# Performance work log

Hardware: AMD Instinct MI355X
Metric: run time of the kernel (lower is better)

The kernel has to match this reference:

```python
import jax, jax.numpy as jnp
import numpy as np

MARGIN = 1.0


def setup_inputs() -> dict:
    key = jax.random.key(0)
    k1, k2 = jax.random.split(key)
    N, D, C = 8192, 128, 64
    embeddings = jax.random.normal(k1, (N, D), dtype=jnp.float32)
    labels = jax.random.randint(k2, (N,), 0, C, dtype=jnp.int64)
    return {"embeddings": embeddings, "labels": labels}


def _pairwise_euclidean(x):
    # ||xi - xj|| via Gram trick; safe sqrt (zero grad at 0, matches masked use)
    sq = jnp.sum(x * x, axis=1)                      # [N]
    d2 = sq[:, None] + sq[None, :] - 2.0 * (x @ x.T)  # [N, N]
    d2 = jnp.maximum(d2, 0.0)
    pos = d2 > 0.0
    return jnp.where(pos, jnp.sqrt(jnp.where(pos, d2, 1.0)), 0.0)


def reference(embeddings, labels):
    N = embeddings.shape[0]
    dist = _pairwise_euclidean(embeddings)            # [N, N]
    same = labels[:, None] == labels[None, :]         # [N, N]
    eye = jnp.eye(N, dtype=bool)
    pos_mask = same & ~eye
    neg_mask = ~same

    neg_inf = jnp.float32(-jnp.inf)
    pos_inf = jnp.float32(jnp.inf)
    hardest_pos = jnp.max(jnp.where(pos_mask, dist, neg_inf), axis=1)  # [N]
    hardest_neg = jnp.min(jnp.where(neg_mask, dist, pos_inf), axis=1)  # [N]

    has_pos = jnp.any(pos_mask, axis=1)
    has_neg = jnp.any(neg_mask, axis=1)
    tl = jax.nn.relu(hardest_pos - hardest_neg + MARGIN)               # [N]
    valid = has_pos & has_neg & (tl > 0.0)

    total = jnp.sum(jnp.where(valid, tl, 0.0))
    count = jnp.sum(valid)
    return jnp.where(count > 0, total / jnp.maximum(count, 1).astype(total.dtype), jnp.float32(0.0))
```

## Files before the change

### kernel.cpp

```cpp
#include <hip/hip_runtime.h>
#include <hip/hip_bf16.h>
#include <math.h>

#define NN 8192
#define DD 128
#define BM 256
#define BN 64
#define NPART 16
#define JRANGE (NN / NPART)
#define NTILES (JRANGE / BN)

typedef __attribute__((ext_vector_type(8))) short bf16x8;
typedef __attribute__((ext_vector_type(4))) float f32x4;

#define WS_SJC 0
#define WS_HPK 65536
#define WS_HNK (WS_HPK + NN * 4)
#define WS_AB  (WS_HNK + NN * 4)

__device__ __forceinline__ unsigned fkey(float f) {
    unsigned u = __float_as_uint(f);
    return (u & 0x80000000u) ? ~u : (u | 0x80000000u);
}
__device__ __forceinline__ float fkey_inv(unsigned k) {
    unsigned u = (k & 0x80000000u) ? (k ^ 0x80000000u) : ~k;
    return __uint_as_float(u);
}
__device__ __forceinline__ ushort f2bf(float x) {
    __hip_bfloat16 h = __float2bfloat16(x);
    return *reinterpret_cast<ushort*>(&h);
}

__global__ __launch_bounds__(256)
void prepq_k(const float* __restrict__ emb, const int* __restrict__ lab,
             float2* __restrict__ sjc, unsigned* __restrict__ hpK,
             unsigned* __restrict__ hnK, ushort* __restrict__ aB) {
    const int lane = threadIdx.x & 63;
    const int w    = threadIdx.x >> 6;
    const int half = lane >> 5;
    const int l32  = lane & 31;
    const int row  = blockIdx.x * 8 + w * 2 + half;

    float4 v = reinterpret_cast<const float4*>(emb)[row * 32 + l32];
    float s = 0.f;
    s = fmaf(v.x, v.x, s); s = fmaf(v.y, v.y, s);
    s = fmaf(v.z, v.z, s); s = fmaf(v.w, v.w, s);
#pragma unroll
    for (int off = 1; off < 32; off <<= 1) s += __shfl_xor(s, off, 64);

    ushort4 b;
    b.x = f2bf(v.x); b.y = f2bf(v.y); b.z = f2bf(v.z); b.w = f2bf(v.w);
    const int idx = (row >> 4) * 2048 + (l32 >> 3) * 512 + ((l32 >> 1) & 3) * 128
                  + (row & 15) * 8 + (l32 & 1) * 4;
    *reinterpret_cast<ushort4*>(aB + idx) = b;

    if (l32 == 0) sjc[row] = make_float2(s, __int_as_float(lab[row]));
    if (threadIdx.x < 8) {
        int r0 = blockIdx.x * 8 + threadIdx.x;
        hpK[r0] = 0x007FFFFFu;
        hnK[r0] = 0xFF800000u;
    }
}

__global__ __launch_bounds__(256, 2)
void hardest_k(const ushort* __restrict__ aB, const float2* __restrict__ sjc,
               unsigned* __restrict__ hpK, unsigned* __restrict__ hnK) {
    const int tid  = threadIdx.x;
    const int w    = tid >> 6;
    const int lane = tid & 63;
    const int lrow = lane & 15;
    const int lk   = lane >> 4;
    const int ib   = (int)blockIdx.x >> 4;
    const int part = (int)blockIdx.x & 15;
    const int i0   = ib * BM;
    const int jbeg = part * JRANGE;

    bf16x8 a[4][4];
#pragma unroll
    for (int s = 0; s < 4; ++s) {
        const int gA = ib * 16 + w * 4 + s;
#pragma unroll
        for (int q = 0; q < 4; ++q)
            a[s][q] = *reinterpret_cast<const bf16x8*>(&aB[gA * 2048 + q * 512 + lane * 8]);
    }
    int   li[4][4];
    float hpg[4][4], hng[4][4];
#pragma unroll
    for (int s = 0; s < 4; ++s)
#pragma unroll
        for (int t = 0; t < 4; ++t) {
            float2 md = sjc[i0 + w * 64 + s * 16 + lk * 4 + t];
            li[s][t]  = __float_as_int(md.y);
            hpg[s][t] = -INFINITY;
            hng[s][t] =  INFINITY;
        }

#pragma unroll 2
    for (int jt = 0; jt < NTILES; ++jt) {
        const int j0 = jbeg + jt * BN;
#pragma unroll
        for (int c = 0; c < 4; ++c) {
            const int gB = (j0 >> 4) + c;
            const ushort* bp = &aB[gB * 2048 + lane * 8];
            bf16x8 b0 = *reinterpret_cast<const bf16x8*>(bp);
            bf16x8 b1 = *reinterpret_cast<const bf16x8*>(bp + 512);
            bf16x8 b2 = *reinterpret_cast<const bf16x8*>(bp + 1024);
            bf16x8 b3 = *reinterpret_cast<const bf16x8*>(bp + 1536);
            float2 sv = sjc[j0 + c * 16 + lrow];
            f32x4 acc[4];
            f32x4 zero = {0.f, 0.f, 0.f, 0.f};
#pragma unroll
            for (int s = 0; s < 4; ++s) acc[s] = zero;
            __builtin_amdgcn_s_setprio(1);
#pragma unroll
            for (int s = 0; s < 4; ++s) {
                acc[s] = __builtin_amdgcn_mfma_f32_16x16x32_bf16(a[s][0], b0, acc[s], 0, 0, 0);
                acc[s] = __builtin_amdgcn_mfma_f32_16x16x32_bf16(a[s][1], b1, acc[s], 0, 0, 0);
                acc[s] = __builtin_amdgcn_mfma_f32_16x16x32_bf16(a[s][2], b2, acc[s], 0, 0, 0);
                acc[s] = __builtin_amdgcn_mfma_f32_16x16x32_bf16(a[s][3], b3, acc[s], 0, 0, 0);
            }
            __builtin_amdgcn_s_setprio(0);
            const float sqj = sv.x;
            const int   lj  = __float_as_int(sv.y);
#pragma unroll
            for (int s = 0; s < 4; ++s)
#pragma unroll
                for (int t = 0; t < 4; ++t) {
                    float gg = fmaf(-2.f, acc[s][t], sqj);
                    bool same = (li[s][t] == lj);
                    hpg[s][t] = fmaxf(hpg[s][t], same ? gg : -INFINITY);
                    hng[s][t] = fminf(hng[s][t], same ? INFINITY : gg);
                }
        }
    }

#pragma unroll
    for (int off = 1; off < 16; off <<= 1)
#pragma unroll
        for (int s = 0; s < 4; ++s)
#pragma unroll
            for (int t = 0; t < 4; ++t) {
                hpg[s][t] = fmaxf(hpg[s][t], __shfl_xor(hpg[s][t], off, 64));
                hng[s][t] = fminf(hng[s][t], __shfl_xor(hng[s][t], off, 64));
            }
    if (lrow == 0) {
#pragma unroll
        for (int s = 0; s < 4; ++s)
#pragma unroll
            for (int t = 0; t < 4; ++t) {
                int i = i0 + w * 64 + s * 16 + lk * 4 + t;
                atomicMax(&hpK[i], fkey(hpg[s][t]));
                atomicMin(&hnK[i], fkey(hng[s][t]));
            }
    }
}

__global__ __launch_bounds__(1024)
void final_k(const unsigned* __restrict__ hpK, const unsigned* __restrict__ hnK,
             const float2* __restrict__ sjc, float* __restrict__ out) {
    float total = 0.f, cnt = 0.f;
    for (int i = threadIdx.x; i < NN; i += 1024) {
        float hp = fkey_inv(hpK[i]);
        float hn = fkey_inv(hnK[i]);
        float s  = sjc[i].x;
        float hp2 = s + hp, hn2 = s + hn;
        float hpd = (hp2 == -INFINITY) ? -INFINITY : sqrtf(fmaxf(hp2, 0.f));
        float hnd = (hn2 ==  INFINITY) ?  INFINITY : sqrtf(fmaxf(hn2, 0.f));
        float tl = hpd - hnd + 1.0f;
        if (tl > 0.f) { total += tl; cnt += 1.f; }
    }
#pragma unroll
    for (int off = 1; off < 64; off <<= 1) {
        total += __shfl_xor(total, off, 64);
        cnt   += __shfl_xor(cnt,   off, 64);
    }
    __shared__ float sT[16], sC[16];
    int wave = threadIdx.x >> 6;
    if ((threadIdx.x & 63) == 0) { sT[wave] = total; sC[wave] = cnt; }
    __syncthreads();
    if (threadIdx.x == 0) {
        float T = 0.f, Cn = 0.f;
#pragma unroll
        for (int k = 0; k < 16; ++k) { T += sT[k]; Cn += sC[k]; }
        out[0] = (Cn > 0.f) ? T / Cn : 0.f;
    }
}

extern "C" void kernel_launch(void* const* d_in, const int* in_sizes, int n_in,
                              void* d_out, int out_size, void* d_ws, size_t ws_size,
                              hipStream_t stream) {
    const float* emb = (const float*)d_in[0];
    const int*   lab = (const int*)d_in[1];
    char* ws = (char*)d_ws;
    float2*   sjc = (float2*)(ws + WS_SJC);
    unsigned* hpK = (unsigned*)(ws + WS_HPK);
    unsigned* hnK = (unsigned*)(ws + WS_HNK);
    ushort*   aB  = (ushort*)(ws + WS_AB);

    prepq_k<<<dim3(NN / 8), dim3(256), 0, stream>>>(emb, lab, sjc, hpK, hnK, aB);
    hardest_k<<<dim3((NN / BM) * NPART), dim3(256), 0, stream>>>(aB, sjc, hpK, hnK);
    final_k<<<dim3(1), dim3(1024), 0, stream>>>(hpK, hnK, sjc, (float*)d_out);
}
```

Measured before the change: 39.38 us.

## Stage B tiles through LDS with double-buffered async global_load_lds

```diff
diff --git a/kernel.cpp b/kernel.cpp
--- a/kernel.cpp
+++ b/kernel.cpp
@@ -65,6 +65,9 @@
 __global__ __launch_bounds__(256, 2)
 void hardest_k(const ushort* __restrict__ aB, const float2* __restrict__ sjc,
                unsigned* __restrict__ hpK, unsigned* __restrict__ hnK) {
+    __shared__ __align__(16) ushort Bt[2][4][4][512];
+    __shared__ __align__(16) float2 sjcL[JRANGE];
+
     const int tid  = threadIdx.x;
     const int w    = tid >> 6;
     const int lane = tid & 63;
@@ -75,6 +78,23 @@
     const int i0   = ib * BM;
     const int jbeg = part * JRANGE;
 
+    {
+        const float2* src = sjc + jbeg + w * 128 + lane * 2;
+        __builtin_amdgcn_global_load_lds(
+            (const __attribute__((address_space(1))) uint32_t*)src,
+            (__attribute__((address_space(3))) uint32_t*)&sjcL[w * 128], 16, 0, 0);
+    }
+#define STAGE(BUF, JT) { \
+        const int gB_ = part * 32 + (JT) * 4 + w; \
+        _Pragma("unroll") \
+        for (int q = 0; q < 4; ++q) { \
+            const ushort* g_ = aB + gB_ * 2048 + q * 512 + lane * 8; \
+            __builtin_amdgcn_global_load_lds( \
+                (const __attribute__((address_space(1))) uint32_t*)g_, \
+                (__attribute__((address_space(3))) uint32_t*)&Bt[BUF][w][q][0], 16, 0, 0); \
+        } }
+    STAGE(0, 0)
+
     bf16x8 a[4][4];
 #pragma unroll
     for (int s = 0; s < 4; ++s) {
@@ -95,18 +115,28 @@
             hng[s][t] =  INFINITY;
         }
 
-#pragma unroll 2
+    asm volatile("s_waitcnt vmcnt(0)" ::: "memory");
+    __builtin_amdgcn_s_barrier();
+
+#pragma unroll 1
     for (int jt = 0; jt < NTILES; ++jt) {
-        const int j0 = jbeg + jt * BN;
+        const int cur = jt & 1;
+        __builtin_amdgcn_sched_barrier(0);
+        if (jt + 1 < NTILES) {
+            if (cur == 0) { STAGE(1, jt + 1) } else { STAGE(0, jt + 1) }
+            asm volatile("s_waitcnt vmcnt(4)" ::: "memory");
+        } else {
+            asm volatile("s_waitcnt vmcnt(0)" ::: "memory");
+        }
+        __builtin_amdgcn_s_barrier();
+
 #pragma unroll
         for (int c = 0; c < 4; ++c) {
-            const int gB = (j0 >> 4) + c;
-            const ushort* bp = &aB[gB * 2048 + lane * 8];
-            bf16x8 b0 = *reinterpret_cast<const bf16x8*>(bp);
-            bf16x8 b1 = *reinterpret_cast<const bf16x8*>(bp + 512);
-            bf16x8 b2 = *reinterpret_cast<const bf16x8*>(bp + 1024);
-            bf16x8 b3 = *reinterpret_cast<const bf16x8*>(bp + 1536);
-            float2 sv = sjc[j0 + c * 16 + lrow];
+            bf16x8 b0 = *reinterpret_cast<const bf16x8*>(&Bt[cur][c][0][lane * 8]);
+            bf16x8 b1 = *reinterpret_cast<const bf16x8*>(&Bt[cur][c][1][lane * 8]);
+            bf16x8 b2 = *reinterpret_cast<const bf16x8*>(&Bt[cur][c][2][lane * 8]);
+            bf16x8 b3 = *reinterpret_cast<const bf16x8*>(&Bt[cur][c][3][lane * 8]);
+            float2 sv = sjcL[jt * 64 + c * 16 + lrow];
             f32x4 acc[4];
             f32x4 zero = {0.f, 0.f, 0.f, 0.f};
 #pragma unroll
@@ -132,7 +162,9 @@
                     hng[s][t] = fminf(hng[s][t], same ? INFINITY : gg);
                 }
         }
-    }
+        __builtin_amdgcn_s_barrier();
+    }
+#undef STAGE
 
 #pragma unroll
     for (int off = 1; off < 16; off <<= 1)
```

Measured after the change: 39.66 us. Within noise of the previous version (+0.7%).
